# Kernel tuning notes

Measured on AMD Instinct MI355X. Metric: run time of the kernel, lower is better.

The kernel has to match this reference:

```python
import jax, jax.numpy as jnp
import numpy as np
import math

N_NODES = 50000
N_EDGES = 640000
IN_FEATS = 128
HEADS = 8
OUT_FEATS = 16
D_FF = 4 * IN_FEATS


def setup_inputs() -> dict:
    key = jax.random.key(0)
    ks = jax.random.split(key, 10)
    s = 0.05
    return {
        "feat": jax.random.normal(ks[0], (N_NODES, IN_FEATS), jnp.float32),
        "src": jax.random.randint(ks[1], (N_EDGES,), 0, N_NODES, jnp.int32),
        "dst": jax.random.randint(ks[2], (N_EDGES,), 0, N_NODES, jnp.int32),
        "Wq": jax.random.normal(ks[3], (IN_FEATS, HEADS * OUT_FEATS), jnp.float32) * s,
        "Wk": jax.random.normal(ks[4], (IN_FEATS, HEADS * OUT_FEATS), jnp.float32) * s,
        "Wv": jax.random.normal(ks[5], (IN_FEATS, HEADS * OUT_FEATS), jnp.float32) * s,
        "ln1_g": jnp.ones((IN_FEATS,), jnp.float32),
        "ln1_b": jnp.zeros((IN_FEATS,), jnp.float32),
        "W1": jax.random.normal(ks[6], (IN_FEATS, D_FF), jnp.float32) * s,
        "b1": jnp.zeros((D_FF,), jnp.float32),
        "prelu_a": jnp.full((D_FF,), 0.25, jnp.float32),  # torch PReLU default init
        "W2": jax.random.normal(ks[7], (D_FF, IN_FEATS), jnp.float32) * s,
        "b2": jnp.zeros((IN_FEATS,), jnp.float32),
    }


def layer_norm(x, g, b, eps=1e-5):
    mu = jnp.mean(x, axis=-1, keepdims=True)
    var = jnp.mean(jnp.square(x - mu), axis=-1, keepdims=True)
    return (x - mu) * jax.lax.rsqrt(var + eps) * g + b


def reference(feat, src, dst, Wq, Wk, Wv, ln1_g, ln1_b, W1, b1, prelu_a, W2, b2):
    N = feat.shape[0]
    feat_c = jax.lax.stop_gradient(feat)  # feat.clone().detach()
    q = (feat @ Wq).reshape(N, HEADS, OUT_FEATS)
    k = (feat_c @ Wk).reshape(N, HEADS, OUT_FEATS)
    v = (feat_c @ Wv).reshape(N, HEADS, OUT_FEATS)

    # edge score: dot(k[src], q[dst]) per head -> [E, H]
    e = jnp.einsum('ehd,ehd->eh', k[src], q[dst]) / math.sqrt(OUT_FEATS * HEADS)

    # segment softmax over incoming edges of each dst node
    m = jax.ops.segment_max(e, dst, num_segments=N)          # [N, H]
    e_exp = jnp.exp(e - m[dst])                              # [E, H]
    denom = jax.ops.segment_sum(e_exp, dst, num_segments=N)  # [N, H]
    a = e_exp / denom[dst]                                   # [E, H]

    # weighted scatter-sum aggregation
    msg = v[src] * a[:, :, None]                             # [E, H, D]
    ft2 = jax.ops.segment_sum(msg, dst, num_segments=N)      # [N, H, D]

    rst = ft2.reshape(feat.shape) + feat
    # NOTE: original applies ln1 twice (ln2 is unused) -- reproduced faithfully
    rst = layer_norm(rst, ln1_g, ln1_b)
    h = rst @ W1 + b1
    h = jnp.where(h >= 0, h, prelu_a * h)                    # PReLU, per-channel
    ffn = h @ W2 + b2
    rst = layer_norm(rst + ffn, ln1_g, ln1_b)
    return rst
```

## Files before the change

kernel.cpp:

```cpp
#include <hip/hip_runtime.h>

#define N_NODES 50000
#define N_EDGES 640000
#define F 128
#define DFF 512
#define NB 196

using u32 = unsigned int;
using u16 = unsigned short;

typedef __bf16 bf16x8 __attribute__((ext_vector_type(8)));
typedef float f32x4 __attribute__((ext_vector_type(4)));

__device__ __forceinline__ float bf2f(u16 u) {
    return __uint_as_float(((u32)u) << 16);
}
__device__ __forceinline__ float blo(u32 p) { return __uint_as_float(p << 16); }
__device__ __forceinline__ float bhi(u32 p) { return __uint_as_float(p & 0xffff0000u); }
__device__ __forceinline__ u16 f2bf(float f) {
    u32 u = __float_as_uint(f);
    u += 0x7fffu + ((u >> 16) & 1u);
    return (u16)(u >> 16);
}
__device__ __forceinline__ u32 pack2(float a, float b) {
    return (u32)f2bf(a) | ((u32)f2bf(b) << 16);
}

__global__ void k_hist(const int* __restrict__ dst, int* __restrict__ cnt) {
    int e = blockIdx.x * 256 + threadIdx.x;
    if (e < N_EDGES) atomicAdd(&cnt[dst[e]], 1);
}

__global__ void k_bsum(const int* __restrict__ counts, int* __restrict__ bsum) {
    int i = blockIdx.x * 256 + threadIdx.x;
    int v = (i < N_NODES) ? counts[i] : 0;
#pragma unroll
    for (int off = 32; off >= 1; off >>= 1) v += __shfl_xor(v, off, 64);
    __shared__ int ws[4];
    int lane = threadIdx.x & 63, wid = threadIdx.x >> 6;
    if (lane == 0) ws[wid] = v;
    __syncthreads();
    if (threadIdx.x == 0) bsum[blockIdx.x] = ws[0] + ws[1] + ws[2] + ws[3];
}

__global__ void k_bfill(const int* __restrict__ counts, const int* __restrict__ bsum,
                        int* __restrict__ row_ptr) {
    const int b = blockIdx.x, t = threadIdx.x;
    const int lane = t & 63, wid = t >> 6;
    __shared__ int wsum[4];
    __shared__ int ws[4];

    int bv = (t < b) ? bsum[t] : 0;
#pragma unroll
    for (int off = 32; off >= 1; off >>= 1) bv += __shfl_xor(bv, off, 64);
    if (lane == 0) wsum[wid] = bv;
    __syncthreads();
    const int boff = wsum[0] + wsum[1] + wsum[2] + wsum[3];

    int i = b * 256 + t;
    int v = (i < N_NODES) ? counts[i] : 0;
    int incl = v;
#pragma unroll
    for (int off = 1; off < 64; off <<= 1) {
        int u = __shfl_up(incl, off, 64);
        if (lane >= off) incl += u;
    }
    if (lane == 63) ws[wid] = incl;
    __syncthreads();
    int wo = 0;
#pragma unroll
    for (int j = 0; j < 4; ++j) if (j < wid) wo += ws[j];
    if (i < N_NODES) row_ptr[i] = boff + wo + incl - v;
    if (i == 0) row_ptr[N_NODES] = N_EDGES;
}

__global__ void k_fill(const int* __restrict__ src, const int* __restrict__ dst,
                       const int* __restrict__ row_ptr, int* __restrict__ counts,
                       int* __restrict__ csr_src) {
    int e = blockIdx.x * 256 + threadIdx.x;
    if (e < N_EDGES) {
        int d = dst[e];
        int old = atomicSub(&counts[d], 1);
        csr_src[row_ptr[d + 1] - old] = src[e];
    }
}

#define FEAT_UNITS (N_NODES * F / 4)
#define CNT_UNITS  ((N_NODES + 3) / 4)
__global__ void k_prep(const float* __restrict__ feat, u16* __restrict__ featb,
                       const float* __restrict__ Wq, const float* __restrict__ Wk,
                       const float* __restrict__ Wv, const float* __restrict__ W1,
                       const float* __restrict__ W2, u16* __restrict__ WT,
                       int* __restrict__ counts) {
    int idx = blockIdx.x * 256 + threadIdx.x;
    if (idx < FEAT_UNITS) {
        float4 v = reinterpret_cast<const float4*>(feat)[idx];
        uint2 p;
        p.x = pack2(v.x, v.y);
        p.y = pack2(v.z, v.w);
        reinterpret_cast<uint2*>(featb)[idx] = p;
        return;
    }
    int wi = idx - FEAT_UNITS;
    if (wi < 49152) {
        int mi = wi >> 14;
        int local = wi & 16383;
        const float* W = (mi == 0) ? Wq : ((mi == 1) ? Wk : Wv);
        int n = local >> 7, k = local & 127;
        WT[wi] = f2bf(W[(size_t)k * 128 + n]);
    } else if (wi < 114688) {
        int local = wi - 49152;
        int n = local >> 7, k = local & 127;
        WT[wi] = f2bf(W1[(size_t)k * 512 + n]);
    } else if (wi < 180224) {
        int local = wi - 114688;
        int n = local >> 9, k = local & 511;
        WT[wi] = f2bf(W2[(size_t)k * 128 + n]);
    } else if (wi < 180224 + CNT_UNITS) {
        reinterpret_cast<int4*>(counts)[wi - 180224] = make_int4(0, 0, 0, 0);
    }
}

template <int EPI>
__global__ __launch_bounds__(256) void k_mm(
    const u16* __restrict__ A, int lda,
    const u16* __restrict__ BT,
    void* __restrict__ Cv, int ldc,
    int K,
    const float* __restrict__ bias,
    const float* __restrict__ prelu,
    const u16* __restrict__ resid,
    const float* __restrict__ g,
    const float* __restrict__ bb)
{
    __shared__ u16 smem[17408];
    u16* sA = smem;
    u16* sB = smem + 128 * 64;
    u16* sC = smem;

    const int t = threadIdx.x;
    const int w = t >> 6;
    const int lane = t & 63;
    const int ln = lane & 15, q4 = lane >> 4;
    const int row0 = blockIdx.x * 128;
    const int cb = blockIdx.y * 128;

    f32x4 acc[2][8];
#pragma unroll
    for (int mt = 0; mt < 2; ++mt)
#pragma unroll
        for (int nt = 0; nt < 8; ++nt)
            acc[mt][nt] = (f32x4){0.f, 0.f, 0.f, 0.f};

    uint4 pa[4], pb[4];
#define LOAD_A(kc)                                                             \
    {                                                                          \
        _Pragma("unroll") for (int i = 0; i < 4; ++i) {                        \
            int u = i * 256 + t, r = u >> 3, k8 = (u & 7) * 8;                 \
            int row = row0 + r;                                                \
            uint4 val = make_uint4(0, 0, 0, 0);                                \
            if (row < N_NODES)                                                 \
                val = *reinterpret_cast<const uint4*>(A + (size_t)row * lda + (kc) + k8); \
            pa[i] = val;                                                       \
        }                                                                      \
    }
#define LOAD_B(kc)                                                             \
    {                                                                          \
        _Pragma("unroll") for (int i = 0; i < 4; ++i) {                        \
            int u = i * 256 + t, r = u >> 3, k8 = (u & 7) * 8;                 \
            pb[i] = *reinterpret_cast<const uint4*>(BT + (size_t)(cb + r) * K + (kc) + k8); \
        }                                                                      \
    }

    LOAD_A(0);
    LOAD_B(0);

    for (int kc = 0; kc < K; kc += 64) {
#pragma unroll
        for (int i = 0; i < 4; ++i) {
            int u = i * 256 + t, r = u >> 3, gi = u & 7;
            int off = (r * 8 + (gi ^ (r & 7))) * 8;
            *reinterpret_cast<uint4*>(&sA[off]) = pa[i];
            *reinterpret_cast<uint4*>(&sB[off]) = pb[i];
        }
        __syncthreads();
        if (kc + 64 < K) {
            LOAD_A(kc + 64);
            LOAD_B(kc + 64);
        }
#pragma unroll
        for (int ks = 0; ks < 2; ++ks) {
            const int gsw = ks * 4 + q4;
            const int rA0 = w * 32 + ln;
            const int rA1 = rA0 + 16;
            bf16x8 a0 = *reinterpret_cast<const bf16x8*>(&sA[(rA0 * 8 + (gsw ^ (rA0 & 7))) * 8]);
            bf16x8 a1 = *reinterpret_cast<const bf16x8*>(&sA[(rA1 * 8 + (gsw ^ (rA1 & 7))) * 8]);
#pragma unroll
            for (int nt = 0; nt < 8; ++nt) {
                const int rB = nt * 16 + ln;
                bf16x8 b = *reinterpret_cast<const bf16x8*>(&sB[(rB * 8 + (gsw ^ (rB & 7))) * 8]);
                acc[0][nt] = __builtin_amdgcn_mfma_f32_16x16x32_bf16(a0, b, acc[0][nt], 0, 0, 0);
                acc[1][nt] = __builtin_amdgcn_mfma_f32_16x16x32_bf16(a1, b, acc[1][nt], 0, 0, 0);
            }
        }
        __syncthreads();
    }
#undef LOAD_A
#undef LOAD_B

    if (EPI == 0 || EPI == 1) {
        float bs[8], pr[8];
        if (EPI == 1) {
#pragma unroll
            for (int nt = 0; nt < 8; ++nt) {
                int col = cb + nt * 16 + ln;
                bs[nt] = bias[col];
                pr[nt] = prelu[col];
            }
        }
#pragma unroll
        for (int mt = 0; mt < 2; ++mt)
#pragma unroll
            for (int nt = 0; nt < 8; ++nt)
#pragma unroll
                for (int j = 0; j < 4; ++j) {
                    float x = acc[mt][nt][j];
                    if (EPI == 1) {
                        x += bs[nt];
                        x = (x >= 0.f) ? x : pr[nt] * x;
                    }
                    sC[(w * 32 + mt * 16 + q4 * 4 + j) * 136 + nt * 16 + ln] = f2bf(x);
                }
        __syncthreads();
        u16* C = (u16*)Cv;
#pragma unroll
        for (int i = 0; i < 8; ++i) {
            int u = i * 256 + t;
            int r = u >> 4, c8 = (u & 15) * 8;
            int row = row0 + r;
            if (row < N_NODES) {
                uint4 val = *reinterpret_cast<const uint4*>(&sC[r * 136 + c8]);
                *reinterpret_cast<uint4*>(&C[(size_t)row * ldc + cb + c8]) = val;
            }
        }
    } else {
        float* C = (float*)Cv;
        float bs[8], gv[8], bv[8];
#pragma unroll
        for (int nt = 0; nt < 8; ++nt) {
            int col = nt * 16 + ln;
            bs[nt] = bias[col];
            gv[nt] = g[col];
            bv[nt] = bb[col];
        }
#pragma unroll
        for (int mt = 0; mt < 2; ++mt)
#pragma unroll
            for (int j = 0; j < 4; ++j) {
                int row = row0 + w * 32 + mt * 16 + q4 * 4 + j;
                bool ok = row < N_NODES;
                float vals[8];
                float s = 0.f, ss = 0.f;
#pragma unroll
                for (int nt = 0; nt < 8; ++nt) {
                    float x = acc[mt][nt][j] + bs[nt];
                    if (ok) x += bf2f(resid[(size_t)row * 128 + nt * 16 + ln]);
                    vals[nt] = x;
                    s += x; ss += x * x;
                }
                s += __shfl_xor(s, 8, 16); ss += __shfl_xor(ss, 8, 16);
                s += __shfl_xor(s, 4, 16); ss += __shfl_xor(ss, 4, 16);
                s += __shfl_xor(s, 2, 16); ss += __shfl_xor(ss, 2, 16);
                s += __shfl_xor(s, 1, 16); ss += __shfl_xor(ss, 1, 16);
                float mu = s * (1.f / 128.f);
                float var = ss * (1.f / 128.f) - mu * mu;
                float rs = rsqrtf(var + 1e-5f);
                if (ok) {
#pragma unroll
                    for (int nt = 0; nt < 8; ++nt)
                        C[(size_t)row * 128 + nt * 16 + ln] =
                            (vals[nt] - mu) * rs * gv[nt] + bv[nt];
                }
            }
    }
}

__global__ __launch_bounds__(256) void k_attn(
    const u32* __restrict__ Q32, const float* __restrict__ feat,
    const int* __restrict__ row_ptr, const int* __restrict__ csr_src,
    const float* __restrict__ g, const float* __restrict__ bb,
    u16* __restrict__ rstb)
{
    const int w = threadIdx.x >> 6;
    const int lane = threadIdx.x & 63;
    const int n = blockIdx.x * 4 + w;
    if (n >= N_NODES) return;
    const float scale = 0.08838834764831845f;

    const u32 qp = Q32[(size_t)n * 192 + lane];
    const float q0 = blo(qp), q1 = bhi(qp);
    const int e0 = row_ptr[n], e1 = row_ptr[n + 1];

    float l = 0.f, a0 = 0.f, a1 = 0.f;
    int e = e0;
    for (; e + 4 <= e1; e += 4) {
        int s0 = csr_src[e], s1 = csr_src[e + 1], s2 = csr_src[e + 2], s3 = csr_src[e + 3];
        u32 kp0 = Q32[(size_t)s0 * 192 + 64 + lane];
        u32 kp1 = Q32[(size_t)s1 * 192 + 64 + lane];
        u32 kp2 = Q32[(size_t)s2 * 192 + 64 + lane];
        u32 kp3 = Q32[(size_t)s3 * 192 + 64 + lane];
        u32 vp0 = Q32[(size_t)s0 * 192 + 128 + lane];
        u32 vp1 = Q32[(size_t)s1 * 192 + 128 + lane];
        u32 vp2 = Q32[(size_t)s2 * 192 + 128 + lane];
        u32 vp3 = Q32[(size_t)s3 * 192 + 128 + lane];
        float p0 = blo(kp0) * q0 + bhi(kp0) * q1;
        float p1 = blo(kp1) * q0 + bhi(kp1) * q1;
        float p2 = blo(kp2) * q0 + bhi(kp2) * q1;
        float p3 = blo(kp3) * q0 + bhi(kp3) * q1;
        p0 += __shfl_xor(p0, 4, 8); p1 += __shfl_xor(p1, 4, 8);
        p2 += __shfl_xor(p2, 4, 8); p3 += __shfl_xor(p3, 4, 8);
        p0 += __shfl_xor(p0, 2, 8); p1 += __shfl_xor(p1, 2, 8);
        p2 += __shfl_xor(p2, 2, 8); p3 += __shfl_xor(p3, 2, 8);
        p0 += __shfl_xor(p0, 1, 8); p1 += __shfl_xor(p1, 1, 8);
        p2 += __shfl_xor(p2, 1, 8); p3 += __shfl_xor(p3, 1, 8);
        float ea = __expf(p0 * scale), eb = __expf(p1 * scale);
        float ec = __expf(p2 * scale), ed = __expf(p3 * scale);
        l += (ea + eb) + (ec + ed);
        a0 += ea * blo(vp0) + eb * blo(vp1) + ec * blo(vp2) + ed * blo(vp3);
        a1 += ea * bhi(vp0) + eb * bhi(vp1) + ec * bhi(vp2) + ed * bhi(vp3);
    }
    for (; e < e1; ++e) {
        int s0 = csr_src[e];
        u32 kp0 = Q32[(size_t)s0 * 192 + 64 + lane];
        u32 vp0 = Q32[(size_t)s0 * 192 + 128 + lane];
        float p0 = blo(kp0) * q0 + bhi(kp0) * q1;
        p0 += __shfl_xor(p0, 4, 8);
        p0 += __shfl_xor(p0, 2, 8);
        p0 += __shfl_xor(p0, 1, 8);
        float ea = __expf(p0 * scale);
        l += ea;
        a0 += ea * blo(vp0);
        a1 += ea * bhi(vp0);
    }
    float inv = (l > 0.f) ? 1.f / l : 0.f;
    const int c2 = lane * 2;
    const float2 fr = *reinterpret_cast<const float2*>(feat + (size_t)n * 128 + c2);
    float x0 = a0 * inv + fr.x;
    float x1 = a1 * inv + fr.y;

    float sum = x0 + x1, sq = x0 * x0 + x1 * x1;
#pragma unroll
    for (int off = 32; off >= 1; off >>= 1) {
        sum += __shfl_xor(sum, off, 64);
        sq += __shfl_xor(sq, off, 64);
    }
    float mu = sum * (1.f / 128.f);
    float var = sq * (1.f / 128.f) - mu * mu;
    float rs = rsqrtf(var + 1e-5f);
    float y0 = (x0 - mu) * rs * g[c2] + bb[c2];
    float y1 = (x1 - mu) * rs * g[c2 + 1] + bb[c2 + 1];
    reinterpret_cast<u32*>(rstb)[(size_t)n * 64 + lane] = pack2(y0, y1);
}

extern "C" void kernel_launch(void* const* d_in, const int* in_sizes, int n_in,
                              void* d_out, int out_size, void* d_ws, size_t ws_size,
                              hipStream_t stream)
{
    const float* feat = (const float*)d_in[0];
    const int* src    = (const int*)d_in[1];
    const int* dst    = (const int*)d_in[2];
    const float* Wq   = (const float*)d_in[3];
    const float* Wk   = (const float*)d_in[4];
    const float* Wv   = (const float*)d_in[5];
    const float* ln_g = (const float*)d_in[6];
    const float* ln_b = (const float*)d_in[7];
    const float* W1   = (const float*)d_in[8];
    const float* b1   = (const float*)d_in[9];
    const float* pa   = (const float*)d_in[10];
    const float* W2   = (const float*)d_in[11];
    const float* b2   = (const float*)d_in[12];

    u16* qkv   = (u16*)d_ws;
    u16* h     = qkv + (size_t)N_NODES * 384;
    u16* featb = h;
    u16* rstb  = h + (size_t)N_NODES * 512;
    u16* WT    = rstb + (size_t)N_NODES * 128;
    u16* BqkvT = WT;
    u16* W1T   = WT + 49152;
    u16* W2T   = WT + 114688;
    int* counts  = (int*)(WT + 180224);
    int* row_ptr = counts + ((N_NODES + 3) & ~3);
    int* csr_src = row_ptr + N_NODES + 1;
    int* bsum    = csr_src + N_EDGES;

    k_prep<<<(FEAT_UNITS + 180224 + CNT_UNITS + 255) / 256, 256, 0, stream>>>(
        feat, featb, Wq, Wk, Wv, W1, W2, WT, counts);

    k_hist<<<(N_EDGES + 255) / 256, 256, 0, stream>>>(dst, counts);
    k_bsum<<<NB, 256, 0, stream>>>(counts, bsum);
    k_bfill<<<NB, 256, 0, stream>>>(counts, bsum, row_ptr);
    k_fill<<<(N_EDGES + 255) / 256, 256, 0, stream>>>(src, dst, row_ptr, counts, csr_src);

    const int MBK = (N_NODES + 127) / 128;

    dim3 gqkv(MBK, 3);
    k_mm<0><<<gqkv, 256, 0, stream>>>(featb, 128, BqkvT, qkv, 384, 128,
                                      nullptr, nullptr, nullptr, nullptr, nullptr);

    k_attn<<<(N_NODES + 3) / 4, 256, 0, stream>>>((const u32*)qkv, feat, row_ptr, csr_src,
                                                  ln_g, ln_b, rstb);

    dim3 gf1(MBK, 4);
    k_mm<1><<<gf1, 256, 0, stream>>>(rstb, 128, W1T, h, 512, 128,
                                     b1, pa, nullptr, nullptr, nullptr);

    dim3 gf2(MBK, 1);
    k_mm<2><<<gf2, 256, 0, stream>>>(h, 512, W2T, d_out, 128, 512,
                                     b2, nullptr, rstb, ln_g, ln_b);
}
```

Baseline: 318.3 us.

## Remap attention wave to process 8 edges in parallel with per-head lanes

Restructures the attention kernel so each wave handles 8 edges at once, with each lane owning one head and one edge slot. Each lane loads its 16-element K and V slices with 128-bit loads instead of one 32-bit word per lane, and computes the dot product locally without intra-head shuffles. Accumulators are combined with cross-edge-slot shuffles at the end. This trades more registers and a final 16-value reduction for fewer serialized iterations and wider memory transactions on the gather.

```diff
diff --git a/kernel.cpp b/kernel.cpp
--- a/kernel.cpp
+++ b/kernel.cpp
@@ -295,71 +295,111 @@
     const int lane = threadIdx.x & 63;
     const int n = blockIdx.x * 4 + w;
     if (n >= N_NODES) return;
+    const int h = lane & 7;
+    const int es = lane >> 3;
     const float scale = 0.08838834764831845f;
 
-    const u32 qp = Q32[(size_t)n * 192 + lane];
-    const float q0 = blo(qp), q1 = bhi(qp);
+    float qf[16];
+    {
+        uint4 qa = *reinterpret_cast<const uint4*>(&Q32[(size_t)n * 192 + h * 8]);
+        uint4 qb = *reinterpret_cast<const uint4*>(&Q32[(size_t)n * 192 + h * 8 + 4]);
+        qf[0] = blo(qa.x); qf[1] = bhi(qa.x); qf[2] = blo(qa.y); qf[3] = bhi(qa.y);
+        qf[4] = blo(qa.z); qf[5] = bhi(qa.z); qf[6] = blo(qa.w); qf[7] = bhi(qa.w);
+        qf[8] = blo(qb.x); qf[9] = bhi(qb.x); qf[10] = blo(qb.y); qf[11] = bhi(qb.y);
+        qf[12] = blo(qb.z); qf[13] = bhi(qb.z); qf[14] = blo(qb.w); qf[15] = bhi(qb.w);
+    }
+
     const int e0 = row_ptr[n], e1 = row_ptr[n + 1];
-
-    float l = 0.f, a0 = 0.f, a1 = 0.f;
-    int e = e0;
-    for (; e + 4 <= e1; e += 4) {
-        int s0 = csr_src[e], s1 = csr_src[e + 1], s2 = csr_src[e + 2], s3 = csr_src[e + 3];
-        u32 kp0 = Q32[(size_t)s0 * 192 + 64 + lane];
-        u32 kp1 = Q32[(size_t)s1 * 192 + 64 + lane];
-        u32 kp2 = Q32[(size_t)s2 * 192 + 64 + lane];
-        u32 kp3 = Q32[(size_t)s3 * 192 + 64 + lane];
-        u32 vp0 = Q32[(size_t)s0 * 192 + 128 + lane];
-        u32 vp1 = Q32[(size_t)s1 * 192 + 128 + lane];
-        u32 vp2 = Q32[(size_t)s2 * 192 + 128 + lane];
-        u32 vp3 = Q32[(size_t)s3 * 192 + 128 + lane];
-        float p0 = blo(kp0) * q0 + bhi(kp0) * q1;
-        float p1 = blo(kp1) * q0 + bhi(kp1) * q1;
-        float p2 = blo(kp2) * q0 + bhi(kp2) * q1;
-        float p3 = blo(kp3) * q0 + bhi(kp3) * q1;
-        p0 += __shfl_xor(p0, 4, 8); p1 += __shfl_xor(p1, 4, 8);
-        p2 += __shfl_xor(p2, 4, 8); p3 += __shfl_xor(p3, 4, 8);
-        p0 += __shfl_xor(p0, 2, 8); p1 += __shfl_xor(p1, 2, 8);
-        p2 += __shfl_xor(p2, 2, 8); p3 += __shfl_xor(p3, 2, 8);
-        p0 += __shfl_xor(p0, 1, 8); p1 += __shfl_xor(p1, 1, 8);
-        p2 += __shfl_xor(p2, 1, 8); p3 += __shfl_xor(p3, 1, 8);
-        float ea = __expf(p0 * scale), eb = __expf(p1 * scale);
-        float ec = __expf(p2 * scale), ed = __expf(p3 * scale);
-        l += (ea + eb) + (ec + ed);
-        a0 += ea * blo(vp0) + eb * blo(vp1) + ec * blo(vp2) + ed * blo(vp3);
-        a1 += ea * bhi(vp0) + eb * bhi(vp1) + ec * bhi(vp2) + ed * bhi(vp3);
-    }
-    for (; e < e1; ++e) {
-        int s0 = csr_src[e];
-        u32 kp0 = Q32[(size_t)s0 * 192 + 64 + lane];
-        u32 vp0 = Q32[(size_t)s0 * 192 + 128 + lane];
-        float p0 = blo(kp0) * q0 + bhi(kp0) * q1;
-        p0 += __shfl_xor(p0, 4, 8);
-        p0 += __shfl_xor(p0, 2, 8);
-        p0 += __shfl_xor(p0, 1, 8);
-        float ea = __expf(p0 * scale);
+    float acc[16];
+#pragma unroll
+    for (int d = 0; d < 16; ++d) acc[d] = 0.f;
+    float l = 0.f;
+
+    for (int eb = e0; eb < e1; eb += 8) {
+        int e = eb + es;
+        bool valid = e < e1;
+        int sn = csr_src[valid ? e : e1 - 1];
+        const u32* base = &Q32[(size_t)sn * 192 + h * 8];
+        uint4 k0 = *reinterpret_cast<const uint4*>(base + 64);
+        uint4 k1 = *reinterpret_cast<const uint4*>(base + 68);
+        uint4 v0 = *reinterpret_cast<const uint4*>(base + 128);
+        uint4 v1 = *reinterpret_cast<const uint4*>(base + 132);
+
+        float p0 = 0.f, p1 = 0.f, p2 = 0.f, p3 = 0.f;
+        p0 = fmaf(blo(k0.x), qf[0], p0);  p1 = fmaf(bhi(k0.x), qf[1], p1);
+        p2 = fmaf(blo(k0.y), qf[2], p2);  p3 = fmaf(bhi(k0.y), qf[3], p3);
+        p0 = fmaf(blo(k0.z), qf[4], p0);  p1 = fmaf(bhi(k0.z), qf[5], p1);
+        p2 = fmaf(blo(k0.w), qf[6], p2);  p3 = fmaf(bhi(k0.w), qf[7], p3);
+        p0 = fmaf(blo(k1.x), qf[8], p0);  p1 = fmaf(bhi(k1.x), qf[9], p1);
+        p2 = fmaf(blo(k1.y), qf[10], p2); p3 = fmaf(bhi(k1.y), qf[11], p3);
+        p0 = fmaf(blo(k1.z), qf[12], p0); p1 = fmaf(bhi(k1.z), qf[13], p1);
+        p2 = fmaf(blo(k1.w), qf[14], p2); p3 = fmaf(bhi(k1.w), qf[15], p3);
+        float p = (p0 + p1) + (p2 + p3);
+
+        float ea = valid ? __expf(p * scale) : 0.f;
         l += ea;
-        a0 += ea * blo(vp0);
-        a1 += ea * bhi(vp0);
+        acc[0]  = fmaf(ea, blo(v0.x), acc[0]);  acc[1]  = fmaf(ea, bhi(v0.x), acc[1]);
+        acc[2]  = fmaf(ea, blo(v0.y), acc[2]);  acc[3]  = fmaf(ea, bhi(v0.y), acc[3]);
+        acc[4]  = fmaf(ea, blo(v0.z), acc[4]);  acc[5]  = fmaf(ea, bhi(v0.z), acc[5]);
+        acc[6]  = fmaf(ea, blo(v0.w), acc[6]);  acc[7]  = fmaf(ea, bhi(v0.w), acc[7]);
+        acc[8]  = fmaf(ea, blo(v1.x), acc[8]);  acc[9]  = fmaf(ea, bhi(v1.x), acc[9]);
+        acc[10] = fmaf(ea, blo(v1.y), acc[10]); acc[11] = fmaf(ea, bhi(v1.y), acc[11]);
+        acc[12] = fmaf(ea, blo(v1.z), acc[12]); acc[13] = fmaf(ea, bhi(v1.z), acc[13]);
+        acc[14] = fmaf(ea, blo(v1.w), acc[14]); acc[15] = fmaf(ea, bhi(v1.w), acc[15]);
+    }
+
+#pragma unroll
+    for (int m = 8; m <= 32; m <<= 1) {
+        l += __shfl_xor(l, m, 64);
+#pragma unroll
+        for (int d = 0; d < 16; ++d) acc[d] += __shfl_xor(acc[d], m, 64);
     }
     float inv = (l > 0.f) ? 1.f / l : 0.f;
-    const int c2 = lane * 2;
-    const float2 fr = *reinterpret_cast<const float2*>(feat + (size_t)n * 128 + c2);
-    float x0 = a0 * inv + fr.x;
-    float x1 = a1 * inv + fr.y;
-
-    float sum = x0 + x1, sq = x0 * x0 + x1 * x1;
-#pragma unroll
-    for (int off = 32; off >= 1; off >>= 1) {
-        sum += __shfl_xor(sum, off, 64);
-        sq += __shfl_xor(sq, off, 64);
-    }
-    float mu = sum * (1.f / 128.f);
-    float var = sq * (1.f / 128.f) - mu * mu;
+
+    float x[16];
+    float s = 0.f, ss = 0.f;
+    const float4* fp = reinterpret_cast<const float4*>(feat + (size_t)n * 128 + h * 16);
+#pragma unroll
+    for (int i = 0; i < 4; ++i) {
+        float4 f4 = fp[i];
+        float a0 = fmaf(acc[4 * i + 0], inv, f4.x);
+        float a1 = fmaf(acc[4 * i + 1], inv, f4.y);
+        float a2 = fmaf(acc[4 * i + 2], inv, f4.z);
+        float a3 = fmaf(acc[4 * i + 3], inv, f4.w);
+        x[4 * i + 0] = a0; x[4 * i + 1] = a1; x[4 * i + 2] = a2; x[4 * i + 3] = a3;
+        s += (a0 + a1) + (a2 + a3);
+        ss += (a0 * a0 + a1 * a1) + (a2 * a2 + a3 * a3);
+    }
+#pragma unroll
+    for (int m = 1; m <= 4; m <<= 1) {
+        s += __shfl_xor(s, m, 64);
+        ss += __shfl_xor(ss, m, 64);
+    }
+    float mu = s * (1.f / 128.f);
+    float var = ss * (1.f / 128.f) - mu * mu;
     float rs = rsqrtf(var + 1e-5f);
-    float y0 = (x0 - mu) * rs * g[c2] + bb[c2];
-    float y1 = (x1 - mu) * rs * g[c2 + 1] + bb[c2 + 1];
-    reinterpret_cast<u32*>(rstb)[(size_t)n * 64 + lane] = pack2(y0, y1);
+
+    if (es == 0) {
+        const float4* gp = reinterpret_cast<const float4*>(g + h * 16);
+        const float4* bp = reinterpret_cast<const float4*>(bb + h * 16);
+        uint4 o0, o1;
+        u32 ww[8];
+#pragma unroll
+        for (int i = 0; i < 4; ++i) {
+            float4 gv = gp[i], bv = bp[i];
+            float y0 = (x[4 * i + 0] - mu) * rs * gv.x + bv.x;
+            float y1 = (x[4 * i + 1] - mu) * rs * gv.y + bv.y;
+            float y2 = (x[4 * i + 2] - mu) * rs * gv.z + bv.z;
+            float y3 = (x[4 * i + 3] - mu) * rs * gv.w + bv.w;
+            ww[2 * i] = pack2(y0, y1);
+            ww[2 * i + 1] = pack2(y2, y3);
+        }
+        o0 = make_uint4(ww[0], ww[1], ww[2], ww[3]);
+        o1 = make_uint4(ww[4], ww[5], ww[6], ww[7]);
+        uint4* outp = reinterpret_cast<uint4*>(rstb + (size_t)n * 128 + h * 16);
+        outp[0] = o0;
+        outp[1] = o1;
+    }
 }
 
 extern "C" void kernel_launch(void* const* d_in, const int* in_sizes, int n_in,
```

Result: no change. 318.0 us (-0.1%).
